# Kernel optimization log

Hardware: AMD Instinct MI355X
Metric: run time of the kernel (lower is better)

The kernel has to match this reference:

```python
import jax, jax.numpy as jnp
import numpy as np

N = 100_000      # nodes
E = 1_600_000    # edges (avg degree 16)
F_IN = 165       # Elliptic node features
HID = 64         # hidden_units
NCLS = 2         # num_classes
NEG_SLOPE = 0.2  # PyG GATConv default


def setup_inputs() -> dict:
    key = jax.random.key(0)
    ks = jax.random.split(key, 9)
    x = jax.random.normal(ks[0], (N, F_IN), jnp.float32)
    edge_index = jax.random.randint(ks[1], (2, E), 0, N, jnp.int32)
    W1 = jax.random.normal(ks[2], (F_IN, HID), jnp.float32) / np.sqrt(F_IN)
    a1_src = jax.random.normal(ks[3], (HID,), jnp.float32) / np.sqrt(HID)
    a1_dst = jax.random.normal(ks[4], (HID,), jnp.float32) / np.sqrt(HID)
    b1 = jnp.zeros((HID,), jnp.float32)
    W2 = jax.random.normal(ks[5], (HID, NCLS), jnp.float32) / np.sqrt(HID)
    a2_src = jax.random.normal(ks[6], (NCLS,), jnp.float32) / np.sqrt(NCLS)
    a2_dst = jax.random.normal(ks[7], (NCLS,), jnp.float32) / np.sqrt(NCLS)
    b2 = jnp.zeros((NCLS,), jnp.float32)
    return {"x": x, "edge_index": edge_index, "W1": W1, "a1_src": a1_src,
            "a1_dst": a1_dst, "b1": b1, "W2": W2, "a2_src": a2_src,
            "a2_dst": a2_dst, "b2": b2}


def gat_layer(x, src, dst, W, a_s, a_d, b, n):
    # h: [N, out]; per-edge attention e_ij = LeakyReLU(a_s.h_j + a_d.h_i)
    h = x @ W
    e = jax.nn.leaky_relu((h @ a_s)[src] + (h @ a_d)[dst], NEG_SLOPE)
    # numerically stable segment softmax over incoming edges of each dst node
    emax = jax.ops.segment_max(e, dst, num_segments=n)
    ee = jnp.exp(e - jax.lax.stop_gradient(emax)[dst])
    denom = jax.ops.segment_sum(ee, dst, num_segments=n)
    alpha = ee / denom[dst]                       # [E_tot]
    out = jax.ops.segment_sum(alpha[:, None] * h[src], dst, num_segments=n)
    return out + b


def reference(x, edge_index, W1, a1_src, a1_dst, b1, W2, a2_src, a2_dst, b2):
    n = x.shape[0]
    loops = jnp.arange(n, dtype=edge_index.dtype)   # PyG add_self_loops=True
    src = jnp.concatenate([edge_index[0], loops])
    dst = jnp.concatenate([edge_index[1], loops])
    h = jax.nn.relu(gat_layer(x, src, dst, W1, a1_src, a1_dst, b1, n))
    # F.dropout(training=False) is identity in eval mode
    out = gat_layer(h, src, dst, W2, a2_src, a2_dst, b2, n)
    return out, edge_index
```

## Files before the change

kernel.cpp:

```cpp
#include <hip/hip_runtime.h>
#include <hip/hip_bf16.h>
#include <math.h>

#define N_NODES 100000
#define N_EDGES 1600000
#define F_IN 165
#define HID 64
#define SLOPE 0.2f

#define NBUCK 196
#define BSHIFT 9
#define BMASK 511
#define NBLK 256
#define CHUNK 6250
#define MSCAN (NBUCK * NBLK)

typedef short short8 __attribute__((ext_vector_type(8)));
typedef float f32x4 __attribute__((ext_vector_type(4)));
typedef float f32x2 __attribute__((ext_vector_type(2)));

__device__ __forceinline__ float lrelu(float x) { return x > 0.f ? x : SLOPE * x; }

__device__ __forceinline__ unsigned short f2bf(float f) {
    unsigned u = __float_as_uint(f);
    u += 0x7FFFu + ((u >> 16) & 1u);
    return (unsigned short)(u >> 16);
}
__device__ __forceinline__ float bflo(unsigned u) { return __uint_as_float(u << 16); }
__device__ __forceinline__ float bfhi(unsigned u) { return __uint_as_float(u & 0xFFFF0000u); }
__device__ __forceinline__ unsigned char f2fp8(float f) {
    return (unsigned char)(__builtin_amdgcn_cvt_pk_fp8_f32(f, f, 0, false) & 0xFF);
}

__global__ __launch_bounds__(256) void k_hist(const int* __restrict__ ei,
                                              int* __restrict__ hist,
                                              float* __restrict__ out_edges,
                                              const float* __restrict__ W1,
                                              unsigned short* __restrict__ Wsw) {
    int blk = blockIdx.x, t = threadIdx.x;
    int idx = blk * 256 + t;
    if (idx < 12288) {
        int j = idx & 7;
        int r = idx >> 3;
        int n = r & 15; r >>= 4;
        int tt = r & 3; r >>= 2;
        int q = r & 3;  int c = r >> 2;
        int k = c * 32 + q * 8 + j;
        int col = tt * 16 + n;
        float v = (k < F_IN) ? W1[k * HID + col] : 0.f;
        Wsw[idx] = f2bf(v);
    }
    __shared__ int h[NBUCK];
    for (int j = t; j < NBUCK; j += 256) h[j] = 0;
    __syncthreads();
    int i0 = blk * CHUNK, i1 = i0 + CHUNK;
    for (int i = i0 + t * 2; i < i1; i += 512) {
        int2 sv = *(const int2*)&ei[i];
        int2 dv = *(const int2*)&ei[N_EDGES + i];
        *(float2*)&out_edges[i] = make_float2((float)sv.x, (float)sv.y);
        *(float2*)&out_edges[N_EDGES + i] = make_float2((float)dv.x, (float)dv.y);
        atomicAdd(&h[dv.x >> BSHIFT], 1);
        atomicAdd(&h[dv.y >> BSHIFT], 1);
    }
    __syncthreads();
    for (int j = t; j < NBUCK; j += 256) hist[j * NBLK + blk] = h[j];
}

#define ASTRIDE 200
__global__ __launch_bounds__(256, 4) void k_gemm1(const float* __restrict__ x,
                                                  const unsigned short* __restrict__ Wsw,
                                                  const float* __restrict__ a1s,
                                                  const float* __restrict__ a1d,
                                                  unsigned char* __restrict__ h1,
                                                  float* __restrict__ s1,
                                                  float* __restrict__ d1) {
    __shared__ unsigned short Ah[64 * ASTRIDE];
    const int tid = threadIdx.x;
    const int base = blockIdx.x * 64;

    for (int i = tid; i < 64 * 35; i += 256) {
        int nl = i / 35, kk = 165 + (i - nl * 35);
        Ah[nl * ASTRIDE + kk] = 0;
    }
    const int fbase = base * F_IN;
    const int flim = N_NODES * F_IN;
    for (int i = tid; i < (64 * F_IN) / 4; i += 256) {
        int f = fbase + i * 4;
        float vv[4];
        if (f + 4 <= flim) {
            float4 v = *(const float4*)&x[f];
            vv[0] = v.x; vv[1] = v.y; vv[2] = v.z; vv[3] = v.w;
        } else {
#pragma unroll
            for (int e = 0; e < 4; e++) vv[e] = (f + e < flim) ? x[f + e] : 0.f;
        }
#pragma unroll
        for (int e = 0; e < 4; e++) {
            int g = f + e;
            int node = g / F_IN;
            int kk = g - node * F_IN;
            Ah[(node - base) * ASTRIDE + kk] = f2bf(vv[e]);
        }
    }
    __syncthreads();

    const int lane = tid & 63;
    const int w = tid >> 6;
    const int m16 = lane & 15;
    const int q = lane >> 4;
    f32x4 acc[4];
#pragma unroll
    for (int t = 0; t < 4; t++) acc[t] = (f32x4){0.f, 0.f, 0.f, 0.f};

    const unsigned short* arow = &Ah[(w * 16 + m16) * ASTRIDE];
    const short8* Wsw8 = (const short8*)Wsw;
#pragma unroll
    for (int c = 0; c < 6; c++) {
        short8 a = *(const short8*)&arow[c * 32 + q * 8];
#pragma unroll
        for (int t = 0; t < 4; t++) {
            short8 b = Wsw8[(c * 4 + q) * 64 + t * 16 + m16];
            acc[t] = __builtin_amdgcn_mfma_f32_16x16x32_bf16(a, b, acc[t], 0, 0, 0);
        }
    }

    float as_l[4], ad_l[4];
#pragma unroll
    for (int t = 0; t < 4; t++) { as_l[t] = a1s[t * 16 + m16]; ad_l[t] = a1d[t * 16 + m16]; }
#pragma unroll
    for (int r = 0; r < 4; r++) {
        int node = base + w * 16 + q * 4 + r;
        bool ok = node < N_NODES;
        float ps = 0.f, pd = 0.f;
#pragma unroll
        for (int t = 0; t < 4; t++) {
            float v = acc[t][r];
            if (ok) h1[(size_t)node * HID + t * 16 + m16] = f2fp8(v);
            ps += v * as_l[t];
            pd += v * ad_l[t];
        }
#pragma unroll
        for (int off = 1; off < 16; off <<= 1) {
            ps += __shfl_xor(ps, off);
            pd += __shfl_xor(pd, off);
        }
        if (ok && m16 == 0) { s1[node] = ps; d1[node] = pd; }
    }
}

__global__ void k_scan1(int* __restrict__ a, int* __restrict__ bsum) {
    __shared__ int sd[256];
    int i = blockIdx.x * 256 + threadIdx.x;
    int v = a[i];
    sd[threadIdx.x] = v;
    __syncthreads();
    for (int off = 1; off < 256; off <<= 1) {
        int t = (threadIdx.x >= off) ? sd[threadIdx.x - off] : 0;
        __syncthreads();
        sd[threadIdx.x] += t;
        __syncthreads();
    }
    a[i] = sd[threadIdx.x] - v;
    if (threadIdx.x == 255) bsum[blockIdx.x] = sd[255];
}

__global__ void k_scan2(int* __restrict__ bsum, int nb) {
    __shared__ int sd[256];
    int t = threadIdx.x;
    int v = (t < nb) ? bsum[t] : 0;
    sd[t] = v;
    __syncthreads();
    for (int off = 1; off < 256; off <<= 1) {
        int u = (t >= off) ? sd[t - off] : 0;
        __syncthreads();
        sd[t] += u;
        __syncthreads();
    }
    if (t < nb) bsum[t] = sd[t] - v;
}

__global__ __launch_bounds__(256) void k_part(const int* __restrict__ ei,
                                              const int* __restrict__ off,
                                              const int* __restrict__ bsum,
                                              unsigned* __restrict__ pairs) {
    __shared__ int base_s[NBUCK];
    __shared__ int cnt[NBUCK];
    int blk = blockIdx.x, t = threadIdx.x;
    for (int j = t; j < NBUCK; j += 256) {
        base_s[j] = off[j * NBLK + blk] + bsum[j];
        cnt[j] = 0;
    }
    __syncthreads();
    int i0 = blk * CHUNK, i1 = i0 + CHUNK;
    for (int i = i0 + t * 2; i < i1; i += 512) {
        int2 sv = *(const int2*)&ei[i];
        int2 dv = *(const int2*)&ei[N_EDGES + i];
        int b0 = dv.x >> BSHIFT;
        int p0 = base_s[b0] + atomicAdd(&cnt[b0], 1);
        pairs[p0] = ((unsigned)sv.x << BSHIFT) | (unsigned)(dv.x & BMASK);
        int b1v = dv.y >> BSHIFT;
        int p1 = base_s[b1v] + atomicAdd(&cnt[b1v], 1);
        pairs[p1] = ((unsigned)sv.y << BSHIFT) | (unsigned)(dv.y & BMASK);
    }
}

__global__ __launch_bounds__(512) void k_build2(const unsigned* __restrict__ pairs,
                                                const int* __restrict__ off,
                                                const int* __restrict__ bsum,
                                                int* __restrict__ row_ptr,
                                                int* __restrict__ deg,
                                                int* __restrict__ csr) {
    __shared__ int hcnt[512];
    __shared__ int cur[512];
    int b = blockIdx.x, t = threadIdx.x;
    hcnt[t] = 0;
    __syncthreads();
    int rs = off[b * NBLK] + bsum[b];
    int re = (b == NBUCK - 1) ? N_EDGES : off[(b + 1) * NBLK] + bsum[b + 1];
    for (int j = rs + t; j < re; j += 512)
        atomicAdd(&hcnt[pairs[j] & BMASK], 1);
    __syncthreads();
    int v = hcnt[t];
    cur[t] = v;
    __syncthreads();
    for (int o = 1; o < 512; o <<= 1) {
        int u = (t >= o) ? cur[t - o] : 0;
        __syncthreads();
        cur[t] += u;
        __syncthreads();
    }
    int excl = cur[t] - v;
    __syncthreads();
    cur[t] = rs + excl;
    int node = b * 512 + t;
    if (node < N_NODES) {
        row_ptr[node] = rs + excl;
        deg[node] = v;
    }
    __syncthreads();
    for (int j = rs + t; j < re; j += 512) {
        unsigned p = pairs[j];
        int pos = atomicAdd(&cur[p & BMASK], 1);
        csr[pos] = (int)(p >> BSHIFT);
    }
}

__global__ __launch_bounds__(256, 8) void k_agg1(const unsigned char* __restrict__ h1,
                                                 const float* __restrict__ s1,
                                                 const float* __restrict__ d1,
                                                 const int* __restrict__ row_ptr,
                                                 const int* __restrict__ deg,
                                                 const int* __restrict__ csr,
                                                 const float* __restrict__ b1,
                                                 const float* __restrict__ W2,
                                                 const float* __restrict__ a2s,
                                                 const float* __restrict__ a2d,
                                                 uint2* __restrict__ node2,
                                                 float* __restrict__ d2arr) {
    int gwid = (blockIdx.x * blockDim.x + threadIdx.x) >> 6;
    int lane = threadIdx.x & 63;
    int node = gwid * 4 + (lane >> 4);
    int cg = lane & 15;
    if (node >= N_NODES) return;
    float di = d1[node];
    int rs = row_ptr[node], re = rs + deg[node];
    float dpart = 0.f;
    float4 acc = make_float4(0.f, 0.f, 0.f, 0.f);
    const unsigned char* hb = h1 + cg * 4;

    for (int j0 = rs; j0 < re; j0 += 8) {
        int sv[8]; float ev[8];
#pragma unroll
        for (int k = 0; k < 8; k++) {
            int jk = j0 + k;
            int jc = jk < re ? jk : (re - 1);
            sv[k] = csr[jc];
            float e = __expf(lrelu(s1[sv[k]] + di));
            ev[k] = (jk < re) ? e : 0.f;
        }
        unsigned uv[8];
#pragma unroll
        for (int k = 0; k < 8; k++)
            uv[k] = *(const unsigned*)&hb[(size_t)sv[k] << 6];
#pragma unroll
        for (int k = 0; k < 8; k++) {
            f32x2 lo = __builtin_amdgcn_cvt_pk_f32_fp8((int)uv[k], false);
            f32x2 hi = __builtin_amdgcn_cvt_pk_f32_fp8((int)uv[k], true);
            dpart += ev[k];
            acc.x += ev[k] * lo.x; acc.y += ev[k] * lo.y;
            acc.z += ev[k] * hi.x; acc.w += ev[k] * hi.y;
        }
    }

    float ees = __expf(lrelu(s1[node] + di));
    unsigned us = *(const unsigned*)&hb[(size_t)node << 6];
    f32x2 slo = __builtin_amdgcn_cvt_pk_f32_fp8((int)us, false);
    f32x2 shi = __builtin_amdgcn_cvt_pk_f32_fp8((int)us, true);
    float denom = dpart + ees;
    acc.x += ees * slo.x; acc.y += ees * slo.y;
    acc.z += ees * shi.x; acc.w += ees * shi.y;
    float inv = 1.f / denom;
    float4 bb = *(const float4*)&b1[cg * 4];
    float o0 = fmaxf(acc.x * inv + bb.x, 0.f);
    float o1 = fmaxf(acc.y * inv + bb.y, 0.f);
    float o2 = fmaxf(acc.z * inv + bb.z, 0.f);
    float o3 = fmaxf(acc.w * inv + bb.w, 0.f);
    float2 w0 = *(const float2*)&W2[(cg * 4 + 0) * 2];
    float2 w1 = *(const float2*)&W2[(cg * 4 + 1) * 2];
    float2 w2 = *(const float2*)&W2[(cg * 4 + 2) * 2];
    float2 w3 = *(const float2*)&W2[(cg * 4 + 3) * 2];
    float p0 = o0 * w0.x + o1 * w1.x + o2 * w2.x + o3 * w3.x;
    float p1 = o0 * w0.y + o1 * w1.y + o2 * w2.y + o3 * w3.y;
#pragma unroll
    for (int off = 1; off < 16; off <<= 1) {
        p0 += __shfl_xor(p0, off);
        p1 += __shfl_xor(p1, off);
    }
    if (cg == 0) {
        float s2 = p0 * a2s[0] + p1 * a2s[1];
        float d2v = p0 * a2d[0] + p1 * a2d[1];
        unsigned pk = (unsigned)f2bf(p0) | ((unsigned)f2bf(p1) << 16);
        node2[node] = make_uint2(pk, __float_as_uint(s2));
        d2arr[node] = d2v;
    }
}

__global__ __launch_bounds__(256) void k_agg2(const uint2* __restrict__ node2,
                                              const float* __restrict__ d2arr,
                                              const int* __restrict__ row_ptr,
                                              const int* __restrict__ deg,
                                              const int* __restrict__ csr,
                                              const float* __restrict__ b2,
                                              float* __restrict__ out) {
    int wid = (blockIdx.x * blockDim.x + threadIdx.x) >> 6;
    int lane = threadIdx.x & 63;
    int node = wid * 4 + (lane >> 4);
    int eg = lane & 15;
    if (node >= N_NODES) return;
    uint2 vi = node2[node];
    float d2 = d2arr[node];
    float denom = 0.f, p0 = 0.f, p1 = 0.f;
    int rs = row_ptr[node], re = rs + deg[node];
    for (int j = rs + eg; j < re; j += 16) {
        int s = csr[j];
        uint2 v = node2[s];
        float ee = __expf(lrelu(__uint_as_float(v.y) + d2));
        denom += ee;
        p0 += ee * bflo(v.x);
        p1 += ee * bfhi(v.x);
    }
#pragma unroll
    for (int off = 1; off < 16; off <<= 1) {
        denom += __shfl_xor(denom, off);
        p0 += __shfl_xor(p0, off);
        p1 += __shfl_xor(p1, off);
    }
    if (eg == 0) {
        float ee = __expf(lrelu(__uint_as_float(vi.y) + d2));
        denom += ee;
        p0 += ee * bflo(vi.x);
        p1 += ee * bfhi(vi.x);
        out[(size_t)node * 2 + 0] = p0 / denom + b2[0];
        out[(size_t)node * 2 + 1] = p1 / denom + b2[1];
    }
}

extern "C" void kernel_launch(void* const* d_in, const int* in_sizes, int n_in,
                              void* d_out, int out_size, void* d_ws, size_t ws_size,
                              hipStream_t stream) {
    const float* x   = (const float*)d_in[0];
    const int*   ei  = (const int*)d_in[1];
    const float* W1  = (const float*)d_in[2];
    const float* a1s = (const float*)d_in[3];
    const float* a1d = (const float*)d_in[4];
    const float* b1  = (const float*)d_in[5];
    const float* W2  = (const float*)d_in[6];
    const float* a2s = (const float*)d_in[7];
    const float* a2d = (const float*)d_in[8];
    const float* b2  = (const float*)d_in[9];
    float* out = (float*)d_out;

    unsigned char* h1 = (unsigned char*)d_ws;
    float* s1      = (float*)(h1 + (size_t)N_NODES * HID);
    float* d1      = s1 + N_NODES;
    float* d2arr   = d1 + N_NODES;
    uint2* node2   = (uint2*)(d2arr + N_NODES);
    int* row_ptr   = (int*)(node2 + N_NODES);
    int* deg       = row_ptr + N_NODES;
    int* off       = deg + N_NODES;
    int* bsum      = off + MSCAN + 64;
    int* csr       = bsum + 256;
    unsigned* pairs = (unsigned*)(csr + N_EDGES);
    unsigned short* Wsw = (unsigned short*)(pairs + N_EDGES);

    k_hist<<<NBLK, 256, 0, stream>>>(ei, off, out + 2 * N_NODES, W1, Wsw);
    k_gemm1<<<(N_NODES + 63) / 64, 256, 0, stream>>>(x, Wsw, a1s, a1d, h1, s1, d1);
    k_scan1<<<MSCAN / 256, 256, 0, stream>>>(off, bsum);
    k_scan2<<<1, 256, 0, stream>>>(bsum, MSCAN / 256);
    k_part<<<NBLK, 256, 0, stream>>>(ei, off, bsum, pairs);
    k_build2<<<NBUCK, 512, 0, stream>>>(pairs, off, bsum, row_ptr, deg, csr);
    k_agg1<<<(N_NODES + 15) / 16, 256, 0, stream>>>(h1, s1, d1, row_ptr, deg, csr,
                                                    b1, W2, a2s, a2d, node2, d2arr);
    k_agg2<<<(N_NODES + 15) / 16, 256, 0, stream>>>(node2, d2arr, row_ptr, deg, csr, b2, out);
}
```

Baseline: 210.8 us.

## Strength-reduce gemm1 staging indices, widen agg1 batching, halve agg2 lanes per node

In gemm1, the per-element divide by F_IN during the x-to-LDS staging is replaced by incrementally tracked node/column indices, and the bounds check is skipped for full tiles. agg1 now gathers 16 neighbours per batch instead of 8, which raises memory-level parallelism. Its occupancy hint drops from 8 to 6 to leave room for the extra registers. agg2 assigns 8 lanes per node, each handling two edges per iteration, so a block covers twice as many nodes and the shuffle reduction is shorter.

```diff
diff --git a/kernel.cpp b/kernel.cpp
--- a/kernel.cpp
+++ b/kernel.cpp
@@ -77,6 +77,7 @@
     __shared__ unsigned short Ah[64 * ASTRIDE];
     const int tid = threadIdx.x;
     const int base = blockIdx.x * 64;
+    const bool full = (base + 64 <= N_NODES);
 
     for (int i = tid; i < 64 * 35; i += 256) {
         int nl = i / 35, kk = 165 + (i - nl * 35);
@@ -84,22 +85,33 @@
     }
     const int fbase = base * F_IN;
     const int flim = N_NODES * F_IN;
-    for (int i = tid; i < (64 * F_IN) / 4; i += 256) {
-        int f = fbase + i * 4;
-        float vv[4];
-        if (f + 4 <= flim) {
-            float4 v = *(const float4*)&x[f];
-            vv[0] = v.x; vv[1] = v.y; vv[2] = v.z; vv[3] = v.w;
-        } else {
-#pragma unroll
-            for (int e = 0; e < 4; e++) vv[e] = (f + e < flim) ? x[f + e] : 0.f;
-        }
-#pragma unroll
-        for (int e = 0; e < 4; e++) {
-            int g = f + e;
-            int node = g / F_IN;
-            int kk = g - node * F_IN;
-            Ah[(node - base) * ASTRIDE + kk] = f2bf(vv[e]);
+    {
+        int i4 = tid * 4;
+        int nl = i4 / F_IN;
+        int kk = i4 - nl * F_IN;
+#pragma unroll
+        for (int it = 0; it < 11; it++) {
+            if (i4 < 64 * F_IN) {
+                int f = fbase + i4;
+                float vv[4];
+                if (full || f + 4 <= flim) {
+                    float4 v = *(const float4*)&x[f];
+                    vv[0] = v.x; vv[1] = v.y; vv[2] = v.z; vv[3] = v.w;
+                } else {
+#pragma unroll
+                    for (int e = 0; e < 4; e++) vv[e] = (f + e < flim) ? x[f + e] : 0.f;
+                }
+                int n0 = nl, k0 = kk;
+#pragma unroll
+                for (int e = 0; e < 4; e++) {
+                    Ah[n0 * ASTRIDE + k0] = f2bf(vv[e]);
+                    k0++;
+                    if (k0 == F_IN) { k0 = 0; n0++; }
+                }
+            }
+            i4 += 1024;
+            nl += 6; kk += 34;
+            if (kk >= F_IN) { kk -= F_IN; nl++; }
         }
     }
     __syncthreads();
@@ -245,7 +257,7 @@
     }
 }
 
-__global__ __launch_bounds__(256, 8) void k_agg1(const unsigned char* __restrict__ h1,
+__global__ __launch_bounds__(256, 6) void k_agg1(const unsigned char* __restrict__ h1,
                                                  const float* __restrict__ s1,
                                                  const float* __restrict__ d1,
                                                  const int* __restrict__ row_ptr,
@@ -268,22 +280,22 @@
     float4 acc = make_float4(0.f, 0.f, 0.f, 0.f);
     const unsigned char* hb = h1 + cg * 4;
 
-    for (int j0 = rs; j0 < re; j0 += 8) {
-        int sv[8]; float ev[8];
-#pragma unroll
-        for (int k = 0; k < 8; k++) {
+    for (int j0 = rs; j0 < re; j0 += 16) {
+        int sv[16]; float ev[16];
+#pragma unroll
+        for (int k = 0; k < 16; k++) {
             int jk = j0 + k;
             int jc = jk < re ? jk : (re - 1);
             sv[k] = csr[jc];
             float e = __expf(lrelu(s1[sv[k]] + di));
             ev[k] = (jk < re) ? e : 0.f;
         }
-        unsigned uv[8];
-#pragma unroll
-        for (int k = 0; k < 8; k++)
+        unsigned uv[16];
+#pragma unroll
+        for (int k = 0; k < 16; k++)
             uv[k] = *(const unsigned*)&hb[(size_t)sv[k] << 6];
 #pragma unroll
-        for (int k = 0; k < 8; k++) {
+        for (int k = 0; k < 16; k++) {
             f32x2 lo = __builtin_amdgcn_cvt_pk_f32_fp8((int)uv[k], false);
             f32x2 hi = __builtin_amdgcn_cvt_pk_f32_fp8((int)uv[k], true);
             dpart += ev[k];
@@ -325,32 +337,38 @@
     }
 }
 
-__global__ __launch_bounds__(256) void k_agg2(const uint2* __restrict__ node2,
-                                              const float* __restrict__ d2arr,
-                                              const int* __restrict__ row_ptr,
-                                              const int* __restrict__ deg,
-                                              const int* __restrict__ csr,
-                                              const float* __restrict__ b2,
-                                              float* __restrict__ out) {
+__global__ __launch_bounds__(256, 8) void k_agg2(const uint2* __restrict__ node2,
+                                                 const float* __restrict__ d2arr,
+                                                 const int* __restrict__ row_ptr,
+                                                 const int* __restrict__ deg,
+                                                 const int* __restrict__ csr,
+                                                 const float* __restrict__ b2,
+                                                 float* __restrict__ out) {
     int wid = (blockIdx.x * blockDim.x + threadIdx.x) >> 6;
     int lane = threadIdx.x & 63;
-    int node = wid * 4 + (lane >> 4);
-    int eg = lane & 15;
+    int node = wid * 8 + (lane >> 3);
+    int eg = lane & 7;
     if (node >= N_NODES) return;
     uint2 vi = node2[node];
     float d2 = d2arr[node];
     float denom = 0.f, p0 = 0.f, p1 = 0.f;
     int rs = row_ptr[node], re = rs + deg[node];
     for (int j = rs + eg; j < re; j += 16) {
-        int s = csr[j];
-        uint2 v = node2[s];
-        float ee = __expf(lrelu(__uint_as_float(v.y) + d2));
-        denom += ee;
-        p0 += ee * bflo(v.x);
-        p1 += ee * bfhi(v.x);
-    }
-#pragma unroll
-    for (int off = 1; off < 16; off <<= 1) {
+        int j2 = j + 8;
+        int j2c = j2 < re ? j2 : (re - 1);
+        int sa = csr[j];
+        int sb = csr[j2c];
+        uint2 va = node2[sa];
+        uint2 vb = node2[sb];
+        float ea = __expf(lrelu(__uint_as_float(va.y) + d2));
+        float eb = __expf(lrelu(__uint_as_float(vb.y) + d2));
+        if (j2 >= re) eb = 0.f;
+        denom += ea + eb;
+        p0 += ea * bflo(va.x) + eb * bflo(vb.x);
+        p1 += ea * bfhi(va.x) + eb * bfhi(vb.x);
+    }
+#pragma unroll
+    for (int off = 1; off < 8; off <<= 1) {
         denom += __shfl_xor(denom, off);
         p0 += __shfl_xor(p0, off);
         p1 += __shfl_xor(p1, off);
@@ -401,5 +419,5 @@
     k_build2<<<NBUCK, 512, 0, stream>>>(pairs, off, bsum, row_ptr, deg, csr);
     k_agg1<<<(N_NODES + 15) / 16, 256, 0, stream>>>(h1, s1, d1, row_ptr, deg, csr,
                                                     b1, W2, a2s, a2d, node2, d2arr);
-    k_agg2<<<(N_NODES + 15) / 16, 256, 0, stream>>>(node2, d2arr, row_ptr, deg, csr, b2, out);
-}
+    k_agg2<<<(N_NODES + 31) / 32, 256, 0, stream>>>(node2, d2arr, row_ptr, deg, csr, b2, out);
+}
```

Result: no change. 213.8 us (+1.4%).
